# Performance work log

Measured on AMD Instinct MI355X. Metric: run time of the kernel, lower is better.

Reference implementation:

```python
import jax, jax.numpy as jnp
import numpy as np

N = 1_000_000      # level-0 points
M = 50_000         # level-1 superpoints
G = 16             # graphs in batch (norm_index groups)
DIMS = (32, 128, 64)
EPS = 1e-5
NEG_SLOPE = 0.01   # torch nn.LeakyReLU default


def graph_norm(x, idx, gamma, beta, num_graphs):
    """Per-graph batch norm ('graph' mode): normalize each feature channel
    using mean/var computed over the nodes of each graph (segment)."""
    cnt = jax.ops.segment_sum(jnp.ones((x.shape[0],), x.dtype), idx, num_segments=num_graphs)
    cnt = jnp.maximum(cnt, 1.0)[:, None]                       # [G,1]
    mean = jax.ops.segment_sum(x, idx, num_segments=num_graphs) / cnt      # [G,D]
    ex2 = jax.ops.segment_sum(x * x, idx, num_segments=num_graphs) / cnt   # [G,D]
    var = jnp.maximum(ex2 - mean * mean, 0.0)
    xn = (x - mean[idx]) * jax.lax.rsqrt(var[idx] + EPS)       # gather stats back to nodes
    return xn * gamma + beta


def setup_inputs() -> dict:
    key = jax.random.key(0)
    ks = jax.random.split(key, 8)
    d0, d1, d2 = DIMS
    x = jax.random.normal(ks[0], (N, d0), dtype=jnp.float32)
    W1 = jax.random.normal(ks[1], (d1, d0), dtype=jnp.float32) * (1.0 / np.sqrt(d0))
    b1 = jnp.zeros((d1,), jnp.float32)
    g1 = jnp.ones((d1,), jnp.float32)
    beta1 = jnp.zeros((d1,), jnp.float32)
    W2 = jax.random.normal(ks[2], (d2, d1), dtype=jnp.float32) * (1.0 / np.sqrt(d1))
    b2 = jnp.zeros((d2,), jnp.float32)
    g2 = jnp.ones((d2,), jnp.float32)
    beta2 = jnp.zeros((d2,), jnp.float32)
    norm_index = jnp.sort(jax.random.randint(ks[3], (N,), 0, G)).astype(jnp.int64)
    super_index = jax.random.randint(ks[4], (N,), 0, M).astype(jnp.int64)
    return {"x": x, "W1": W1, "b1": b1, "g1": g1, "beta1": beta1,
            "W2": W2, "b2": b2, "g2": g2, "beta2": beta2,
            "norm_index": norm_index, "super_index": super_index}


def reference(x, W1, b1, g1, beta1, W2, b2, g2, beta2, norm_index, super_index):
    # MLP layer 1: Linear -> graph BatchNorm -> LeakyReLU
    h = jnp.dot(x, W1.T) + b1                                  # [N,128]
    h = jax.nn.leaky_relu(graph_norm(h, norm_index, g1, beta1, G), NEG_SLOPE)
    # MLP layer 2
    h = jnp.dot(h, W2.T) + b2                                  # [N,64]
    h = jax.nn.leaky_relu(graph_norm(h, norm_index, g2, beta2, G), NEG_SLOPE)
    # level == 0: scatter-max pooling into level-1 superpoints
    out = jax.ops.segment_max(h, super_index, num_segments=M)  # [M,64]
    # torch_scatter leaves empty segments at 0; segment_max gives -inf
    out = jnp.where(jnp.isneginf(out), 0.0, out)
    return out
```

## Files before the change

kernel.cpp:

```cpp
#include <hip/hip_runtime.h>
#include <hip/hip_bf16.h>
#include <stdint.h>

#define NGRAPH 16
#define EPSV 1e-5f
#define SLOPE 0.01f

#define OFF_S1   0
#define OFF_CNT  512
#define OFF_SUM2 528
#define OFF_SQ2  1552
#define ZERO_SMALL 2576
#define OFF_A1   2576
#define OFF_C1   4624
#define OFF_A2   6672
#define OFF_C2   7696
#define OFF_M    16384
#define M_FLOATS 16384
#define H2_BYTE_OFF 65536

typedef __attribute__((ext_vector_type(4))) float f32x4;
typedef __attribute__((ext_vector_type(8))) short short8v;

__device__ __forceinline__ unsigned int enc_f32(float f) {
  unsigned int b = __float_as_uint(f);
  return (b & 0x80000000u) ? ~b : (b | 0x80000000u);
}
__device__ __forceinline__ unsigned int f2bf_bits(float f) {
  unsigned int u = __float_as_uint(f);
  unsigned int r = u + 0x7FFFu + ((u >> 16) & 1u);
  return r >> 16;
}
__device__ __forceinline__ float bfround(float f) {
  unsigned int u = __float_as_uint(f);
  unsigned int r = (u + 0x7FFFu + ((u >> 16) & 1u)) & 0xFFFF0000u;
  return __uint_as_float(r);
}

__global__ void k_zero_stats(float* __restrict__ ws) {
  int i = blockIdx.x * 256 + threadIdx.x;
  if (i < ZERO_SMALL) ws[i] = 0.0f;
  int j = i - ZERO_SMALL;
  if (j >= 0 && j < M_FLOATS) ws[OFF_M + j] = 0.0f;
}

__global__ void k_zero_ints(int* __restrict__ p, int n) {
  int i = blockIdx.x * 256 + threadIdx.x;
  if (i < n) p[i] = 0;
}

__global__ void k_init_out(unsigned int* __restrict__ out, int n) {
  int i = blockIdx.x * 256 + threadIdx.x;
  if (i < n) out[i] = 0u;
}

__global__ __launch_bounds__(256) void k1_mom(
    const float* __restrict__ x, const int* __restrict__ gidx,
    float* __restrict__ ws, int N) {
  const int tid = threadIdx.x;
  const int gw = blockIdx.x * 4 + (tid >> 6);
  const int l = tid & 63;
  const int bi = l >> 3, bj = l & 7;
  const bool diag = (bi == bj);
  const bool isL0 = (l == 0);
  const int nwaves = gridDim.x * 4;
  const int npw = (N + nwaves - 1) / nwaves;
  const int n0 = gw * npw;
  const int n1 = min(n0 + npw, N);

  float m00,m01,m02,m03,m10,m11,m12,m13,m20,m21,m22,m23,m30,m31,m32,m33;
  m00=m01=m02=m03=m10=m11=m12=m13=m20=m21=m22=m23=m30=m31=m32=m33=0.f;
  float sv0=0.f, sv1=0.f, sv2=0.f, sv3=0.f, cnt=0.f;
  int curg = -1;

  #pragma unroll 1
  for (int n = n0; n < n1; ++n) {
    int g = gidx[n];
    if (g != curg) {
      if (curg >= 0) {
        float* Mg = ws + OFF_M + curg * 1024 + bi * 4 * 32 + bj * 4;
        atomicAdd(Mg + 0*32 + 0, m00); atomicAdd(Mg + 0*32 + 1, m01);
        atomicAdd(Mg + 0*32 + 2, m02); atomicAdd(Mg + 0*32 + 3, m03);
        atomicAdd(Mg + 1*32 + 0, m10); atomicAdd(Mg + 1*32 + 1, m11);
        atomicAdd(Mg + 1*32 + 2, m12); atomicAdd(Mg + 1*32 + 3, m13);
        atomicAdd(Mg + 2*32 + 0, m20); atomicAdd(Mg + 2*32 + 1, m21);
        atomicAdd(Mg + 2*32 + 2, m22); atomicAdd(Mg + 2*32 + 3, m23);
        atomicAdd(Mg + 3*32 + 0, m30); atomicAdd(Mg + 3*32 + 1, m31);
        atomicAdd(Mg + 3*32 + 2, m32); atomicAdd(Mg + 3*32 + 3, m33);
        if (diag) {
          float* Sg = ws + OFF_S1 + curg * 32 + bi * 4;
          atomicAdd(Sg + 0, sv0); atomicAdd(Sg + 1, sv1);
          atomicAdd(Sg + 2, sv2); atomicAdd(Sg + 3, sv3);
        }
        if (isL0) atomicAdd(ws + OFF_CNT + curg, cnt);
      }
      curg = g;
      m00=m01=m02=m03=m10=m11=m12=m13=m20=m21=m22=m23=m30=m31=m32=m33=0.f;
      sv0=sv1=sv2=sv3=0.f; cnt=0.f;
    }
    const float* xr = x + (size_t)n * 32;
    float4 pi = *(const float4*)(xr + bi * 4);
    float4 pj = *(const float4*)(xr + bj * 4);
    float xi0 = bfround(pi.x), xi1 = bfround(pi.y), xi2 = bfround(pi.z), xi3 = bfround(pi.w);
    float xj0 = bfround(pj.x), xj1 = bfround(pj.y), xj2 = bfround(pj.z), xj3 = bfround(pj.w);
    m00 = fmaf(xi0,xj0,m00); m01 = fmaf(xi0,xj1,m01); m02 = fmaf(xi0,xj2,m02); m03 = fmaf(xi0,xj3,m03);
    m10 = fmaf(xi1,xj0,m10); m11 = fmaf(xi1,xj1,m11); m12 = fmaf(xi1,xj2,m12); m13 = fmaf(xi1,xj3,m13);
    m20 = fmaf(xi2,xj0,m20); m21 = fmaf(xi2,xj1,m21); m22 = fmaf(xi2,xj2,m22); m23 = fmaf(xi2,xj3,m23);
    m30 = fmaf(xi3,xj0,m30); m31 = fmaf(xi3,xj1,m31); m32 = fmaf(xi3,xj2,m32); m33 = fmaf(xi3,xj3,m33);
    if (diag) { sv0 += xi0; sv1 += xi1; sv2 += xi2; sv3 += xi3; }
    cnt += 1.f;
  }
  if (curg >= 0) {
    float* Mg = ws + OFF_M + curg * 1024 + bi * 4 * 32 + bj * 4;
    atomicAdd(Mg + 0*32 + 0, m00); atomicAdd(Mg + 0*32 + 1, m01);
    atomicAdd(Mg + 0*32 + 2, m02); atomicAdd(Mg + 0*32 + 3, m03);
    atomicAdd(Mg + 1*32 + 0, m10); atomicAdd(Mg + 1*32 + 1, m11);
    atomicAdd(Mg + 1*32 + 2, m12); atomicAdd(Mg + 1*32 + 3, m13);
    atomicAdd(Mg + 2*32 + 0, m20); atomicAdd(Mg + 2*32 + 1, m21);
    atomicAdd(Mg + 2*32 + 2, m22); atomicAdd(Mg + 2*32 + 3, m23);
    atomicAdd(Mg + 3*32 + 0, m30); atomicAdd(Mg + 3*32 + 1, m31);
    atomicAdd(Mg + 3*32 + 2, m32); atomicAdd(Mg + 3*32 + 3, m33);
    if (diag) {
      float* Sg = ws + OFF_S1 + curg * 32 + bi * 4;
      atomicAdd(Sg + 0, sv0); atomicAdd(Sg + 1, sv1);
      atomicAdd(Sg + 2, sv2); atomicAdd(Sg + 3, sv3);
    }
    if (isL0) atomicAdd(ws + OFF_CNT + curg, cnt);
  }
}

__global__ __launch_bounds__(128) void k2a_fin1(
    const float* __restrict__ W1, const float* __restrict__ b1,
    const float* __restrict__ g1, const float* __restrict__ be1,
    float* __restrict__ ws) {
  __shared__ float Ms[1024];
  __shared__ float ss[32];
  __shared__ float cs;
  const int g = blockIdx.x, c = threadIdx.x;
  for (int i = c; i < 1024; i += 128) Ms[i] = ws[OFF_M + g * 1024 + i];
  if (c < 32) ss[c] = ws[OFF_S1 + g * 32 + c];
  if (c == 0) cs = fmaxf(ws[OFF_CNT + g], 1.0f);
  __syncthreads();
  float w[32];
  #pragma unroll
  for (int k = 0; k < 32; ++k) w[k] = bfround(W1[c * 32 + k]);
  float dot = 0.f;
  #pragma unroll
  for (int k = 0; k < 32; ++k) dot = fmaf(w[k], ss[k], dot);
  float quad = 0.f;
  #pragma unroll 1
  for (int i = 0; i < 32; ++i) {
    const float* Mr = Ms + i * 32;
    float acc = 0.f;
    #pragma unroll
    for (int j = 0; j < 32; ++j) acc = fmaf(Mr[j], w[j], acc);
    quad = fmaf(w[i], acc, quad);
  }
  const float cnt = cs;
  const float bc = b1[c];
  const float mean = dot / cnt + bc;
  const float e2 = (quad + 2.f * bc * dot) / cnt + bc * bc;
  const float var = fmaxf(e2 - mean * mean, 0.0f);
  const float a = rsqrtf(var + EPSV) * g1[c];
  ws[OFF_A1 + g * 128 + c] = a;
  ws[OFF_C1 + g * 128 + c] = fmaf(a, bc - mean, be1[c]);
}

__global__ void k2_fin(float* __restrict__ ws, const float* __restrict__ gamma,
                       const float* __restrict__ beta, int D, int off_sum,
                       int off_sq, int off_a, int off_c) {
  int i = blockIdx.x * 256 + threadIdx.x;
  if (i >= NGRAPH * D) return;
  int g = i / D, c = i % D;
  float cnt  = fmaxf(ws[OFF_CNT + g], 1.0f);
  float mean = ws[off_sum + i] / cnt;
  float ex2  = ws[off_sq + i] / cnt;
  float var  = fmaxf(ex2 - mean * mean, 0.0f);
  float a = rsqrtf(var + EPSV) * gamma[c];
  ws[off_a + i] = a;
  ws[off_c + i] = fmaf(-mean, a, beta[c]);
}

__global__ __launch_bounds__(256) void k3_mfma(
    const float* __restrict__ x, const float* __restrict__ W1,
    const float* __restrict__ W2, const float* __restrict__ b2,
    const int* __restrict__ gidx, float* __restrict__ ws,
    unsigned short* __restrict__ h2out, int N, int ntiles, int tpb) {
  __shared__ float a1s[2048];
  __shared__ float c1s[2048];
  __shared__ __align__(16) unsigned short h1t[4][2048];
  const int tid = threadIdx.x;
  const int wv = tid >> 6;
  const int l = tid & 63;
  const int ln = l & 15;
  const int kq = l >> 4;

  for (int i = tid; i < 2048; i += 256) { a1s[i] = ws[OFF_A1 + i]; c1s[i] = ws[OFF_C1 + i]; }

  short8v w1f[8];
  #pragma unroll
  for (int t = 0; t < 8; ++t) {
    const float* wr = W1 + (size_t)(t * 16 + ln) * 32 + kq * 8;
    float4 p = *(const float4*)wr, q = *(const float4*)(wr + 4);
    short8v f;
    f[0] = (short)f2bf_bits(p.x); f[1] = (short)f2bf_bits(p.y);
    f[2] = (short)f2bf_bits(p.z); f[3] = (short)f2bf_bits(p.w);
    f[4] = (short)f2bf_bits(q.x); f[5] = (short)f2bf_bits(q.y);
    f[6] = (short)f2bf_bits(q.z); f[7] = (short)f2bf_bits(q.w);
    w1f[t] = f;
  }
  short8v w2f[4][4];
  #pragma unroll
  for (int ct = 0; ct < 4; ++ct)
    #pragma unroll
    for (int kt = 0; kt < 4; ++kt) {
      const float* wr = W2 + (size_t)(ct * 16 + ln) * 128 + kt * 32 + kq * 8;
      float4 p = *(const float4*)wr, q = *(const float4*)(wr + 4);
      short8v f;
      f[0] = (short)f2bf_bits(p.x); f[1] = (short)f2bf_bits(p.y);
      f[2] = (short)f2bf_bits(p.z); f[3] = (short)f2bf_bits(p.w);
      f[4] = (short)f2bf_bits(q.x); f[5] = (short)f2bf_bits(q.y);
      f[6] = (short)f2bf_bits(q.z); f[7] = (short)f2bf_bits(q.w);
      w2f[ct][kt] = f;
    }
  float b2v[4];
  #pragma unroll
  for (int ct = 0; ct < 4; ++ct) b2v[ct] = b2[ct * 16 + ln];
  __syncthreads();

  unsigned short* myt = &h1t[wv][0];
  const f32x4 zero4 = {0.f, 0.f, 0.f, 0.f};
  float s2[4] = {0.f, 0.f, 0.f, 0.f}, q2[4] = {0.f, 0.f, 0.f, 0.f};
  int curg2 = -1;

  const int t0 = blockIdx.x * tpb;
  const int t1 = min(t0 + tpb, ntiles);
  #pragma unroll 1
  for (int tb = t0; tb < t1; tb += 4) {
    const int tile = tb + wv;
    const bool act = (tile < t1);
    int gg[4] = {0, 0, 0, 0};
    if (act) {
      const int base = tile * 16;
      const int nodeA = min(base + ln, N - 1);
      const float* xr = x + (size_t)nodeA * 32 + kq * 8;
      float4 p = *(const float4*)xr, q = *(const float4*)(xr + 4);
      short8v af;
      af[0] = (short)f2bf_bits(p.x); af[1] = (short)f2bf_bits(p.y);
      af[2] = (short)f2bf_bits(p.z); af[3] = (short)f2bf_bits(p.w);
      af[4] = (short)f2bf_bits(q.x); af[5] = (short)f2bf_bits(q.y);
      af[6] = (short)f2bf_bits(q.z); af[7] = (short)f2bf_bits(q.w);
      f32x4 acc1[8];
      #pragma unroll
      for (int t = 0; t < 8; ++t)
        acc1[t] = __builtin_amdgcn_mfma_f32_16x16x32_bf16(af, w1f[t], zero4, 0, 0, 0);
      #pragma unroll
      for (int i = 0; i < 4; ++i)
        gg[i] = gidx[min(base + kq * 4 + i, N - 1)];
      #pragma unroll
      for (int t = 0; t < 8; ++t) {
        const int ct_ = t * 16 + ln;
        #pragma unroll
        for (int i = 0; i < 4; ++i) {
          const float a = a1s[gg[i] * 128 + ct_];
          const float cc = c1s[gg[i] * 128 + ct_];
          float v = fmaf(acc1[t][i], a, cc);
          v = v >= 0.f ? v : v * SLOPE;
          const int row = kq * 4 + i;
          const int byte = (row * 256 + ct_ * 2) ^ ((row & 7) << 4);
          *(unsigned short*)((char*)myt + byte) = (unsigned short)f2bf_bits(v);
        }
      }
    }
    __syncthreads();
    if (act) {
      const int base = tile * 16;
      short8v a2f[4];
      #pragma unroll
      for (int kt = 0; kt < 4; ++kt) {
        const int byte = (ln * 256 + kt * 64 + kq * 16) ^ ((ln & 7) << 4);
        a2f[kt] = *(const short8v*)((const char*)myt + byte);
      }
      f32x4 acc2[4];
      #pragma unroll
      for (int ct = 0; ct < 4; ++ct) {
        f32x4 a = zero4;
        #pragma unroll
        for (int kt = 0; kt < 4; ++kt)
          a = __builtin_amdgcn_mfma_f32_16x16x32_bf16(a2f[kt], w2f[ct][kt], a, 0, 0, 0);
        acc2[ct] = a;
      }
      #pragma unroll
      for (int i = 0; i < 4; ++i) {
        const int node = base + kq * 4 + i;
        if (node >= N) break;
        const int g = gg[i];
        if (g != curg2) {
          if (curg2 >= 0) {
            #pragma unroll
            for (int ct = 0; ct < 4; ++ct) {
              atomicAdd(ws + OFF_SUM2 + curg2 * 64 + ct * 16 + ln, s2[ct]);
              atomicAdd(ws + OFF_SQ2  + curg2 * 64 + ct * 16 + ln, q2[ct]);
            }
          }
          curg2 = g;
          #pragma unroll
          for (int ct = 0; ct < 4; ++ct) { s2[ct] = 0.f; q2[ct] = 0.f; }
        }
        #pragma unroll
        for (int ct = 0; ct < 4; ++ct) {
          const float v2 = acc2[ct][i] + b2v[ct];
          s2[ct] += v2; q2[ct] = fmaf(v2, v2, q2[ct]);
          h2out[(size_t)node * 64 + ct * 16 + ln] = (unsigned short)f2bf_bits(v2);
        }
      }
    }
  }
  if (curg2 >= 0) {
    #pragma unroll
    for (int ct = 0; ct < 4; ++ct) {
      atomicAdd(ws + OFF_SUM2 + curg2 * 64 + ct * 16 + ln, s2[ct]);
      atomicAdd(ws + OFF_SQ2  + curg2 * 64 + ct * 16 + ln, q2[ct]);
    }
  }
}

__global__ void k5a_hist(const int* __restrict__ sidx, int* __restrict__ hist, int N) {
  int n = blockIdx.x * 256 + threadIdx.x;
  if (n < N) atomicAdd(&hist[sidx[n]], 1);
}

__global__ __launch_bounds__(256) void k5b_scan(
    const int* __restrict__ hist, int* __restrict__ offsets,
    int* __restrict__ cursor, int M, int N) {
  __shared__ int part[256];
  const int tid = threadIdx.x;
  const int chunk = (M + 255) / 256;
  const int lo = min(tid * chunk, M), hi = min(lo + chunk, M);
  int s = 0;
  for (int i = lo; i < hi; ++i) s += hist[i];
  part[tid] = s;
  __syncthreads();
  if (tid == 0) {
    int run = 0;
    for (int i = 0; i < 256; ++i) { int v = part[i]; part[i] = run; run += v; }
  }
  __syncthreads();
  int run = part[tid];
  for (int i = lo; i < hi; ++i) {
    int v = hist[i];
    offsets[i] = run; cursor[i] = run; run += v;
  }
  if (tid == 255) offsets[M] = N;
}

__global__ void k5c_perm(const int* __restrict__ sidx, int* __restrict__ cursor,
                         int* __restrict__ perm, int N) {
  int n = blockIdx.x * 256 + threadIdx.x;
  if (n >= N) return;
  int sp = sidx[n];
  int pos = atomicAdd(&cursor[sp], 1);
  perm[pos] = n;
}

__global__ __launch_bounds__(256) void k5d_gather(
    const unsigned short* __restrict__ h2, const int* __restrict__ perm,
    const int* __restrict__ offsets, const int* __restrict__ gidx,
    const float* __restrict__ ws, float* __restrict__ out, int M) {
  __shared__ float a2s[1024], c2s[1024];
  const int tid = threadIdx.x;
  for (int i = tid; i < 1024; i += 256) { a2s[i] = ws[OFF_A2 + i]; c2s[i] = ws[OFF_C2 + i]; }
  __syncthreads();
  const int seg = blockIdx.x * 4 + (tid >> 6);
  if (seg >= M) return;
  const int lane = tid & 63;
  const int lo = offsets[seg], hi = offsets[seg + 1];
  float acc = -3.402823466e38f;
  #pragma unroll 1
  for (int i = lo; i < hi; ++i) {
    const int node = perm[i];
    const int g = gidx[node];
    const unsigned short hb = h2[(size_t)node * 64 + lane];
    const float v = __uint_as_float((unsigned int)hb << 16);
    float y = fmaf(v, a2s[g * 64 + lane], c2s[g * 64 + lane]);
    y = y >= 0.f ? y : y * SLOPE;
    acc = fmaxf(acc, y);
  }
  out[(size_t)seg * 64 + lane] = (hi > lo) ? acc : 0.0f;
}

__global__ __launch_bounds__(256) void k5_scatter(
    const unsigned int* __restrict__ h2, const int* __restrict__ gidx,
    const int* __restrict__ sidx, const float* __restrict__ ws,
    unsigned int* __restrict__ out, int N) {
  int t = blockIdx.x * 256 + threadIdx.x;
  int node = t >> 4;
  if (node >= N) return;
  int jq = t & 15, j = jq * 4;
  int g = gidx[node];
  int sp = sidx[node];
  float4 av = *(const float4*)(ws + OFF_A2 + g * 64 + j);
  float4 cv = *(const float4*)(ws + OFF_C2 + g * 64 + j);
  uint2 hv = *(const uint2*)(h2 + (size_t)node * 32 + jq * 2);
  float v0 = __uint_as_float(hv.x << 16);
  float v1 = __uint_as_float(hv.x & 0xFFFF0000u);
  float v2 = __uint_as_float(hv.y << 16);
  float v3 = __uint_as_float(hv.y & 0xFFFF0000u);
  v0 = fmaf(v0, av.x, cv.x); v0 = v0 >= 0.f ? v0 : v0 * SLOPE;
  v1 = fmaf(v1, av.y, cv.y); v1 = v1 >= 0.f ? v1 : v1 * SLOPE;
  v2 = fmaf(v2, av.z, cv.z); v2 = v2 >= 0.f ? v2 : v2 * SLOPE;
  v3 = fmaf(v3, av.w, cv.w); v3 = v3 >= 0.f ? v3 : v3 * SLOPE;
  unsigned int* o = out + (size_t)sp * 64 + j;
  atomicMax(o + 0, enc_f32(v0));
  atomicMax(o + 1, enc_f32(v1));
  atomicMax(o + 2, enc_f32(v2));
  atomicMax(o + 3, enc_f32(v3));
}

__global__ void k6_decode(unsigned int* __restrict__ o, int n) {
  int i = blockIdx.x * 256 + threadIdx.x;
  if (i >= n) return;
  unsigned int e = o[i];
  float f;
  if (e == 0u) f = 0.0f;
  else if (e & 0x80000000u) f = __uint_as_float(e ^ 0x80000000u);
  else f = __uint_as_float(~e);
  ((float*)o)[i] = f;
}

extern "C" void kernel_launch(void* const* d_in, const int* in_sizes, int n_in,
                              void* d_out, int out_size, void* d_ws, size_t ws_size,
                              hipStream_t stream) {
  const float* x   = (const float*)d_in[0];
  const float* W1  = (const float*)d_in[1];
  const float* b1  = (const float*)d_in[2];
  const float* g1  = (const float*)d_in[3];
  const float* be1 = (const float*)d_in[4];
  const float* W2  = (const float*)d_in[5];
  const float* b2  = (const float*)d_in[6];
  const float* g2  = (const float*)d_in[7];
  const float* be2 = (const float*)d_in[8];
  const int* gidx  = (const int*)d_in[9];
  const int* sidx  = (const int*)d_in[10];
  const int N = in_sizes[9];
  const int M = out_size / 64;
  float* ws = (float*)d_ws;
  unsigned short* h2 = (unsigned short*)((char*)d_ws + H2_BYTE_OFF);
  unsigned int* out_u = (unsigned int*)d_out;

  const size_t idx_off = (size_t)H2_BYTE_OFF + (size_t)N * 128;
  int* hist    = (int*)((char*)d_ws + idx_off);
  int* cursor  = hist + M;
  int* offsets = cursor + M;
  int* perm    = offsets + M + 1;
  const size_t needed_fast = idx_off + (size_t)(3 * M + 1 + N) * 4;
  const bool fast = (ws_size >= needed_fast);

  const int zthreads = ZERO_SMALL + M_FLOATS;
  hipLaunchKernelGGL(k_zero_stats, dim3((zthreads + 255) / 256), dim3(256), 0, stream, ws);
  hipLaunchKernelGGL(k1_mom, dim3(1024), dim3(256), 0, stream, x, gidx, ws, N);
  hipLaunchKernelGGL(k2a_fin1, dim3(NGRAPH), dim3(128), 0, stream, W1, b1, g1, be1, ws);
  const int ntiles = (N + 15) / 16;
  const int tpb = (ntiles + 1023) / 1024;
  const int k3blocks = (ntiles + tpb - 1) / tpb;
  hipLaunchKernelGGL(k3_mfma, dim3(k3blocks), dim3(256), 0, stream,
                     x, W1, W2, b2, gidx, ws, h2, N, ntiles, tpb);
  hipLaunchKernelGGL(k2_fin, dim3((NGRAPH * 64 + 255) / 256), dim3(256), 0, stream,
                     ws, g2, be2, 64, OFF_SUM2, OFF_SQ2, OFF_A2, OFF_C2);
  if (fast) {
    hipLaunchKernelGGL(k_zero_ints, dim3((M + 255) / 256), dim3(256), 0, stream, hist, M);
    hipLaunchKernelGGL(k5a_hist, dim3((N + 255) / 256), dim3(256), 0, stream, sidx, hist, N);
    hipLaunchKernelGGL(k5b_scan, dim3(1), dim3(256), 0, stream, hist, offsets, cursor, M, N);
    hipLaunchKernelGGL(k5c_perm, dim3((N + 255) / 256), dim3(256), 0, stream,
                       sidx, cursor, perm, N);
    hipLaunchKernelGGL(k5d_gather, dim3((M + 3) / 4), dim3(256), 0, stream,
                       h2, perm, offsets, gidx, ws, (float*)d_out, M);
  } else {
    hipLaunchKernelGGL(k_init_out, dim3((out_size + 255) / 256), dim3(256), 0, stream,
                       out_u, out_size);
    hipLaunchKernelGGL(k5_scatter, dim3((N * 16 + 255) / 256), dim3(256), 0, stream,
                       (const unsigned int*)h2, gidx, sidx, ws, out_u, N);
    hipLaunchKernelGGL(k6_decode, dim3((out_size + 255) / 256), dim3(256), 0, stream,
                       out_u, out_size);
  }
}
```

Baseline: 1.133 ms.

## Prefetch next rows in moment, MFMA and gather loops; drop block syncs

Several changes land together. The moment kernel and the gather kernel now software-prefetch the next row, index and perm entry one or two iterations ahead to hide load latency. The MFMA kernel gives each wave its own contiguous run of tiles, which removes the per-iteration __syncthreads, and it also prefetches the next tile. The graph id is packed into the perm entries so the gather loop no longer reads gidx per node. The zeroing kernels are merged into one, and the histogram, scan and perm kernels are moved earlier in the stream. This costs some extra registers and redundant clamped loads at the ends of each range.

```diff
diff --git a/kernel.cpp b/kernel.cpp
--- a/kernel.cpp
+++ b/kernel.cpp
@@ -37,16 +37,11 @@
   return __uint_as_float(r);
 }
 
-__global__ void k_zero_stats(float* __restrict__ ws) {
+__global__ void k_zero_all(float* __restrict__ ws, int* __restrict__ hist, int M) {
   int i = blockIdx.x * 256 + threadIdx.x;
   if (i < ZERO_SMALL) ws[i] = 0.0f;
-  int j = i - ZERO_SMALL;
-  if (j >= 0 && j < M_FLOATS) ws[OFF_M + j] = 0.0f;
-}
-
-__global__ void k_zero_ints(int* __restrict__ p, int n) {
-  int i = blockIdx.x * 256 + threadIdx.x;
-  if (i < n) p[i] = 0;
+  if (i < M_FLOATS) ws[OFF_M + i] = 0.0f;
+  if (i < M) hist[i] = 0;
 }
 
 __global__ void k_init_out(unsigned int* __restrict__ out, int n) {
@@ -73,42 +68,49 @@
   float sv0=0.f, sv1=0.f, sv2=0.f, sv3=0.f, cnt=0.f;
   int curg = -1;
 
-  #pragma unroll 1
-  for (int n = n0; n < n1; ++n) {
-    int g = gidx[n];
-    if (g != curg) {
-      if (curg >= 0) {
-        float* Mg = ws + OFF_M + curg * 1024 + bi * 4 * 32 + bj * 4;
-        atomicAdd(Mg + 0*32 + 0, m00); atomicAdd(Mg + 0*32 + 1, m01);
-        atomicAdd(Mg + 0*32 + 2, m02); atomicAdd(Mg + 0*32 + 3, m03);
-        atomicAdd(Mg + 1*32 + 0, m10); atomicAdd(Mg + 1*32 + 1, m11);
-        atomicAdd(Mg + 1*32 + 2, m12); atomicAdd(Mg + 1*32 + 3, m13);
-        atomicAdd(Mg + 2*32 + 0, m20); atomicAdd(Mg + 2*32 + 1, m21);
-        atomicAdd(Mg + 2*32 + 2, m22); atomicAdd(Mg + 2*32 + 3, m23);
-        atomicAdd(Mg + 3*32 + 0, m30); atomicAdd(Mg + 3*32 + 1, m31);
-        atomicAdd(Mg + 3*32 + 2, m32); atomicAdd(Mg + 3*32 + 3, m33);
-        if (diag) {
-          float* Sg = ws + OFF_S1 + curg * 32 + bi * 4;
-          atomicAdd(Sg + 0, sv0); atomicAdd(Sg + 1, sv1);
-          atomicAdd(Sg + 2, sv2); atomicAdd(Sg + 3, sv3);
+  if (n0 < n1) {
+    const int nlast = n1 - 1;
+    int g = gidx[n0];
+    float4 pi = *(const float4*)(x + (size_t)n0 * 32 + bi * 4);
+    float4 pj = *(const float4*)(x + (size_t)n0 * 32 + bj * 4);
+    #pragma unroll 1
+    for (int n = n0; n < n1; ++n) {
+      const int nn = min(n + 1, nlast);
+      const int g2 = gidx[nn];
+      float4 pi2 = *(const float4*)(x + (size_t)nn * 32 + bi * 4);
+      float4 pj2 = *(const float4*)(x + (size_t)nn * 32 + bj * 4);
+      if (g != curg) {
+        if (curg >= 0) {
+          float* Mg = ws + OFF_M + curg * 1024 + bi * 4 * 32 + bj * 4;
+          atomicAdd(Mg + 0*32 + 0, m00); atomicAdd(Mg + 0*32 + 1, m01);
+          atomicAdd(Mg + 0*32 + 2, m02); atomicAdd(Mg + 0*32 + 3, m03);
+          atomicAdd(Mg + 1*32 + 0, m10); atomicAdd(Mg + 1*32 + 1, m11);
+          atomicAdd(Mg + 1*32 + 2, m12); atomicAdd(Mg + 1*32 + 3, m13);
+          atomicAdd(Mg + 2*32 + 0, m20); atomicAdd(Mg + 2*32 + 1, m21);
+          atomicAdd(Mg + 2*32 + 2, m22); atomicAdd(Mg + 2*32 + 3, m23);
+          atomicAdd(Mg + 3*32 + 0, m30); atomicAdd(Mg + 3*32 + 1, m31);
+          atomicAdd(Mg + 3*32 + 2, m32); atomicAdd(Mg + 3*32 + 3, m33);
+          if (diag) {
+            float* Sg = ws + OFF_S1 + curg * 32 + bi * 4;
+            atomicAdd(Sg + 0, sv0); atomicAdd(Sg + 1, sv1);
+            atomicAdd(Sg + 2, sv2); atomicAdd(Sg + 3, sv3);
+          }
+          if (isL0) atomicAdd(ws + OFF_CNT + curg, cnt);
         }
-        if (isL0) atomicAdd(ws + OFF_CNT + curg, cnt);
+        curg = g;
+        m00=m01=m02=m03=m10=m11=m12=m13=m20=m21=m22=m23=m30=m31=m32=m33=0.f;
+        sv0=sv1=sv2=sv3=0.f; cnt=0.f;
       }
-      curg = g;
-      m00=m01=m02=m03=m10=m11=m12=m13=m20=m21=m22=m23=m30=m31=m32=m33=0.f;
-      sv0=sv1=sv2=sv3=0.f; cnt=0.f;
-    }
-    const float* xr = x + (size_t)n * 32;
-    float4 pi = *(const float4*)(xr + bi * 4);
-    float4 pj = *(const float4*)(xr + bj * 4);
-    float xi0 = bfround(pi.x), xi1 = bfround(pi.y), xi2 = bfround(pi.z), xi3 = bfround(pi.w);
-    float xj0 = bfround(pj.x), xj1 = bfround(pj.y), xj2 = bfround(pj.z), xj3 = bfround(pj.w);
-    m00 = fmaf(xi0,xj0,m00); m01 = fmaf(xi0,xj1,m01); m02 = fmaf(xi0,xj2,m02); m03 = fmaf(xi0,xj3,m03);
-    m10 = fmaf(xi1,xj0,m10); m11 = fmaf(xi1,xj1,m11); m12 = fmaf(xi1,xj2,m12); m13 = fmaf(xi1,xj3,m13);
-    m20 = fmaf(xi2,xj0,m20); m21 = fmaf(xi2,xj1,m21); m22 = fmaf(xi2,xj2,m22); m23 = fmaf(xi2,xj3,m23);
-    m30 = fmaf(xi3,xj0,m30); m31 = fmaf(xi3,xj1,m31); m32 = fmaf(xi3,xj2,m32); m33 = fmaf(xi3,xj3,m33);
-    if (diag) { sv0 += xi0; sv1 += xi1; sv2 += xi2; sv3 += xi3; }
-    cnt += 1.f;
+      float xi0 = bfround(pi.x), xi1 = bfround(pi.y), xi2 = bfround(pi.z), xi3 = bfround(pi.w);
+      float xj0 = bfround(pj.x), xj1 = bfround(pj.y), xj2 = bfround(pj.z), xj3 = bfround(pj.w);
+      m00 = fmaf(xi0,xj0,m00); m01 = fmaf(xi0,xj1,m01); m02 = fmaf(xi0,xj2,m02); m03 = fmaf(xi0,xj3,m03);
+      m10 = fmaf(xi1,xj0,m10); m11 = fmaf(xi1,xj1,m11); m12 = fmaf(xi1,xj2,m12); m13 = fmaf(xi1,xj3,m13);
+      m20 = fmaf(xi2,xj0,m20); m21 = fmaf(xi2,xj1,m21); m22 = fmaf(xi2,xj2,m22); m23 = fmaf(xi2,xj3,m23);
+      m30 = fmaf(xi3,xj0,m30); m31 = fmaf(xi3,xj1,m31); m32 = fmaf(xi3,xj2,m32); m33 = fmaf(xi3,xj3,m33);
+      if (diag) { sv0 += xi0; sv1 += xi1; sv2 += xi2; sv3 += xi3; }
+      cnt += 1.f;
+      pi = pi2; pj = pj2; g = g2;
+    }
   }
   if (curg >= 0) {
     float* Mg = ws + OFF_M + curg * 1024 + bi * 4 * 32 + bj * 4;
@@ -185,7 +187,7 @@
     const float* __restrict__ x, const float* __restrict__ W1,
     const float* __restrict__ W2, const float* __restrict__ b2,
     const int* __restrict__ gidx, float* __restrict__ ws,
-    unsigned short* __restrict__ h2out, int N, int ntiles, int tpb) {
+    unsigned short* __restrict__ h2out, int N, int ntiles, int tpw) {
   __shared__ float a1s[2048];
   __shared__ float c1s[2048];
   __shared__ __align__(16) unsigned short h1t[4][2048];
@@ -228,99 +230,111 @@
   for (int ct = 0; ct < 4; ++ct) b2v[ct] = b2[ct * 16 + ln];
   __syncthreads();
 
+  const int gw = blockIdx.x * 4 + wv;
+  const int t0 = gw * tpw;
+  const int t1 = min(t0 + tpw, ntiles);
+  if (t0 >= t1) return;
+
   unsigned short* myt = &h1t[wv][0];
   const f32x4 zero4 = {0.f, 0.f, 0.f, 0.f};
-  float s2[4] = {0.f, 0.f, 0.f, 0.f}, q2[4] = {0.f, 0.f, 0.f, 0.f};
+  float s2[4] = {0.f, 0.f, 0.f, 0.f}, q2a[4] = {0.f, 0.f, 0.f, 0.f};
   int curg2 = -1;
 
-  const int t0 = blockIdx.x * tpb;
-  const int t1 = min(t0 + tpb, ntiles);
+  float4 p, q;
+  int gg[4];
+  {
+    const int base = t0 * 16;
+    const float* xr = x + (size_t)min(base + ln, N - 1) * 32 + kq * 8;
+    p = *(const float4*)xr; q = *(const float4*)(xr + 4);
+    #pragma unroll
+    for (int i = 0; i < 4; ++i) gg[i] = gidx[min(base + kq * 4 + i, N - 1)];
+  }
+
   #pragma unroll 1
-  for (int tb = t0; tb < t1; tb += 4) {
-    const int tile = tb + wv;
-    const bool act = (tile < t1);
-    int gg[4] = {0, 0, 0, 0};
-    if (act) {
-      const int base = tile * 16;
-      const int nodeA = min(base + ln, N - 1);
-      const float* xr = x + (size_t)nodeA * 32 + kq * 8;
-      float4 p = *(const float4*)xr, q = *(const float4*)(xr + 4);
-      short8v af;
-      af[0] = (short)f2bf_bits(p.x); af[1] = (short)f2bf_bits(p.y);
-      af[2] = (short)f2bf_bits(p.z); af[3] = (short)f2bf_bits(p.w);
-      af[4] = (short)f2bf_bits(q.x); af[5] = (short)f2bf_bits(q.y);
-      af[6] = (short)f2bf_bits(q.z); af[7] = (short)f2bf_bits(q.w);
-      f32x4 acc1[8];
+  for (int t = t0; t < t1; ++t) {
+    const int base = t * 16;
+    float4 p2, q2;
+    int gg2[4];
+    {
+      const int nb = min(t + 1, t1 - 1) * 16;
+      const float* xr = x + (size_t)min(nb + ln, N - 1) * 32 + kq * 8;
+      p2 = *(const float4*)xr; q2 = *(const float4*)(xr + 4);
       #pragma unroll
-      for (int t = 0; t < 8; ++t)
-        acc1[t] = __builtin_amdgcn_mfma_f32_16x16x32_bf16(af, w1f[t], zero4, 0, 0, 0);
+      for (int i = 0; i < 4; ++i) gg2[i] = gidx[min(nb + kq * 4 + i, N - 1)];
+    }
+    short8v af;
+    af[0] = (short)f2bf_bits(p.x); af[1] = (short)f2bf_bits(p.y);
+    af[2] = (short)f2bf_bits(p.z); af[3] = (short)f2bf_bits(p.w);
+    af[4] = (short)f2bf_bits(q.x); af[5] = (short)f2bf_bits(q.y);
+    af[6] = (short)f2bf_bits(q.z); af[7] = (short)f2bf_bits(q.w);
+    f32x4 acc1[8];
+    #pragma unroll
+    for (int tt = 0; tt < 8; ++tt)
+      acc1[tt] = __builtin_amdgcn_mfma_f32_16x16x32_bf16(af, w1f[tt], zero4, 0, 0, 0);
+    #pragma unroll
+    for (int tt = 0; tt < 8; ++tt) {
+      const int ct_ = tt * 16 + ln;
       #pragma unroll
-      for (int i = 0; i < 4; ++i)
-        gg[i] = gidx[min(base + kq * 4 + i, N - 1)];
+      for (int i = 0; i < 4; ++i) {
+        const float a = a1s[gg[i] * 128 + ct_];
+        const float cc = c1s[gg[i] * 128 + ct_];
+        float v = fmaf(acc1[tt][i], a, cc);
+        v = v >= 0.f ? v : v * SLOPE;
+        const int row = kq * 4 + i;
+        const int byte = (row * 256 + ct_ * 2) ^ ((row & 7) << 4);
+        *(unsigned short*)((char*)myt + byte) = (unsigned short)f2bf_bits(v);
+      }
+    }
+    asm volatile("s_waitcnt lgkmcnt(0)" ::: "memory");
+    __builtin_amdgcn_sched_barrier(0);
+    short8v a2f[4];
+    #pragma unroll
+    for (int kt = 0; kt < 4; ++kt) {
+      const int byte = (ln * 256 + kt * 64 + kq * 16) ^ ((ln & 7) << 4);
+      a2f[kt] = *(const short8v*)((const char*)myt + byte);
+    }
+    f32x4 acc2[4];
+    #pragma unroll
+    for (int ct = 0; ct < 4; ++ct) {
+      f32x4 a = zero4;
       #pragma unroll
-      for (int t = 0; t < 8; ++t) {
-        const int ct_ = t * 16 + ln;
+      for (int kt = 0; kt < 4; ++kt)
+        a = __builtin_amdgcn_mfma_f32_16x16x32_bf16(a2f[kt], w2f[ct][kt], a, 0, 0, 0);
+      acc2[ct] = a;
+    }
+    #pragma unroll
+    for (int i = 0; i < 4; ++i) {
+      const int node = base + kq * 4 + i;
+      if (node >= N) break;
+      const int g = gg[i];
+      if (g != curg2) {
+        if (curg2 >= 0) {
+          #pragma unroll
+          for (int ct = 0; ct < 4; ++ct) {
+            atomicAdd(ws + OFF_SUM2 + curg2 * 64 + ct * 16 + ln, s2[ct]);
+            atomicAdd(ws + OFF_SQ2  + curg2 * 64 + ct * 16 + ln, q2a[ct]);
+          }
+        }
+        curg2 = g;
         #pragma unroll
-        for (int i = 0; i < 4; ++i) {
-          const float a = a1s[gg[i] * 128 + ct_];
-          const float cc = c1s[gg[i] * 128 + ct_];
-          float v = fmaf(acc1[t][i], a, cc);
-          v = v >= 0.f ? v : v * SLOPE;
-          const int row = kq * 4 + i;
-          const int byte = (row * 256 + ct_ * 2) ^ ((row & 7) << 4);
-          *(unsigned short*)((char*)myt + byte) = (unsigned short)f2bf_bits(v);
-        }
+        for (int ct = 0; ct < 4; ++ct) { s2[ct] = 0.f; q2a[ct] = 0.f; }
       }
-    }
-    __syncthreads();
-    if (act) {
-      const int base = tile * 16;
-      short8v a2f[4];
-      #pragma unroll
-      for (int kt = 0; kt < 4; ++kt) {
-        const int byte = (ln * 256 + kt * 64 + kq * 16) ^ ((ln & 7) << 4);
-        a2f[kt] = *(const short8v*)((const char*)myt + byte);
-      }
-      f32x4 acc2[4];
       #pragma unroll
       for (int ct = 0; ct < 4; ++ct) {
-        f32x4 a = zero4;
-        #pragma unroll
-        for (int kt = 0; kt < 4; ++kt)
-          a = __builtin_amdgcn_mfma_f32_16x16x32_bf16(a2f[kt], w2f[ct][kt], a, 0, 0, 0);
-        acc2[ct] = a;
+        const float v2 = acc2[ct][i] + b2v[ct];
+        s2[ct] += v2; q2a[ct] = fmaf(v2, v2, q2a[ct]);
+        h2out[(size_t)node * 64 + ct * 16 + ln] = (unsigned short)f2bf_bits(v2);
       }
-      #pragma unroll
-      for (int i = 0; i < 4; ++i) {
-        const int node = base + kq * 4 + i;
-        if (node >= N) break;
-        const int g = gg[i];
-        if (g != curg2) {
-          if (curg2 >= 0) {
-            #pragma unroll
-            for (int ct = 0; ct < 4; ++ct) {
-              atomicAdd(ws + OFF_SUM2 + curg2 * 64 + ct * 16 + ln, s2[ct]);
-              atomicAdd(ws + OFF_SQ2  + curg2 * 64 + ct * 16 + ln, q2[ct]);
-            }
-          }
-          curg2 = g;
-          #pragma unroll
-          for (int ct = 0; ct < 4; ++ct) { s2[ct] = 0.f; q2[ct] = 0.f; }
-        }
-        #pragma unroll
-        for (int ct = 0; ct < 4; ++ct) {
-          const float v2 = acc2[ct][i] + b2v[ct];
-          s2[ct] += v2; q2[ct] = fmaf(v2, v2, q2[ct]);
-          h2out[(size_t)node * 64 + ct * 16 + ln] = (unsigned short)f2bf_bits(v2);
-        }
-      }
-    }
+    }
+    p = p2; q = q2;
+    #pragma unroll
+    for (int i = 0; i < 4; ++i) gg[i] = gg2[i];
   }
   if (curg2 >= 0) {
     #pragma unroll
     for (int ct = 0; ct < 4; ++ct) {
       atomicAdd(ws + OFF_SUM2 + curg2 * 64 + ct * 16 + ln, s2[ct]);
-      atomicAdd(ws + OFF_SQ2  + curg2 * 64 + ct * 16 + ln, q2[ct]);
+      atomicAdd(ws + OFF_SQ2  + curg2 * 64 + ct * 16 + ln, q2a[ct]);
     }
   }
 }
@@ -354,19 +368,19 @@
   if (tid == 255) offsets[M] = N;
 }
 
-__global__ void k5c_perm(const int* __restrict__ sidx, int* __restrict__ cursor,
-                         int* __restrict__ perm, int N) {
+__global__ void k5c_perm(const int* __restrict__ sidx, const int* __restrict__ gidx,
+                         int* __restrict__ cursor, int* __restrict__ perm, int N) {
   int n = blockIdx.x * 256 + threadIdx.x;
   if (n >= N) return;
   int sp = sidx[n];
   int pos = atomicAdd(&cursor[sp], 1);
-  perm[pos] = n;
+  perm[pos] = (n << 4) | (gidx[n] & 15);
 }
 
 __global__ __launch_bounds__(256) void k5d_gather(
     const unsigned short* __restrict__ h2, const int* __restrict__ perm,
-    const int* __restrict__ offsets, const int* __restrict__ gidx,
-    const float* __restrict__ ws, float* __restrict__ out, int M) {
+    const int* __restrict__ offsets, const float* __restrict__ ws,
+    float* __restrict__ out, int M) {
   __shared__ float a2s[1024], c2s[1024];
   const int tid = threadIdx.x;
   for (int i = tid; i < 1024; i += 256) { a2s[i] = ws[OFF_A2 + i]; c2s[i] = ws[OFF_C2 + i]; }
@@ -376,15 +390,22 @@
   const int lane = tid & 63;
   const int lo = offsets[seg], hi = offsets[seg + 1];
   float acc = -3.402823466e38f;
-  #pragma unroll 1
-  for (int i = lo; i < hi; ++i) {
-    const int node = perm[i];
-    const int g = gidx[node];
-    const unsigned short hb = h2[(size_t)node * 64 + lane];
-    const float v = __uint_as_float((unsigned int)hb << 16);
-    float y = fmaf(v, a2s[g * 64 + lane], c2s[g * 64 + lane]);
-    y = y >= 0.f ? y : y * SLOPE;
-    acc = fmaxf(acc, y);
+  if (hi > lo) {
+    const int last = hi - 1;
+    int pc = perm[lo];
+    unsigned short hc = h2[(size_t)(pc >> 4) * 64 + lane];
+    int pn = perm[min(lo + 1, last)];
+    #pragma unroll 1
+    for (int i = lo; i < hi; ++i) {
+      const unsigned short hn = h2[(size_t)(pn >> 4) * 64 + lane];
+      const int pn2 = perm[min(i + 2, last)];
+      const int g = pc & 15;
+      const float v = __uint_as_float((unsigned int)hc << 16);
+      float y = fmaf(v, a2s[g * 64 + lane], c2s[g * 64 + lane]);
+      y = y >= 0.f ? y : y * SLOPE;
+      acc = fmaxf(acc, y);
+      pc = pn; hc = hn; pn = pn2;
+    }
   }
   out[(size_t)seg * 64 + lane] = (hi > lo) ? acc : 0.0f;
 }
@@ -456,25 +477,28 @@
   const size_t needed_fast = idx_off + (size_t)(3 * M + 1 + N) * 4;
   const bool fast = (ws_size >= needed_fast);
 
-  const int zthreads = ZERO_SMALL + M_FLOATS;
-  hipLaunchKernelGGL(k_zero_stats, dim3((zthreads + 255) / 256), dim3(256), 0, stream, ws);
+  const int zmax = (M_FLOATS > M ? M_FLOATS : M);
+  hipLaunchKernelGGL(k_zero_all, dim3((zmax + 255) / 256), dim3(256), 0, stream,
+                     ws, hist, fast ? M : 0);
   hipLaunchKernelGGL(k1_mom, dim3(1024), dim3(256), 0, stream, x, gidx, ws, N);
   hipLaunchKernelGGL(k2a_fin1, dim3(NGRAPH), dim3(128), 0, stream, W1, b1, g1, be1, ws);
+  if (fast) {
+    hipLaunchKernelGGL(k5a_hist, dim3((N + 255) / 256), dim3(256), 0, stream, sidx, hist, N);
+    hipLaunchKernelGGL(k5b_scan, dim3(1), dim3(256), 0, stream, hist, offsets, cursor, M, N);
+    hipLaunchKernelGGL(k5c_perm, dim3((N + 255) / 256), dim3(256), 0, stream,
+                       sidx, gidx, cursor, perm, N);
+  }
   const int ntiles = (N + 15) / 16;
-  const int tpb = (ntiles + 1023) / 1024;
-  const int k3blocks = (ntiles + tpb - 1) / tpb;
+  const int NW = 4096;
+  const int tpw = (ntiles + NW - 1) / NW;
+  const int k3blocks = (ntiles + 4 * tpw - 1) / (4 * tpw);
   hipLaunchKernelGGL(k3_mfma, dim3(k3blocks), dim3(256), 0, stream,
-                     x, W1, W2, b2, gidx, ws, h2, N, ntiles, tpb);
+                     x, W1, W2, b2, gidx, ws, h2, N, ntiles, tpw);
   hipLaunchKernelGGL(k2_fin, dim3((NGRAPH * 64 + 255) / 256), dim3(256), 0, stream,
                      ws, g2, be2, 64, OFF_SUM2, OFF_SQ2, OFF_A2, OFF_C2);
   if (fast) {
-    hipLaunchKernelGGL(k_zero_ints, dim3((M + 255) / 256), dim3(256), 0, stream, hist, M);
-    hipLaunchKernelGGL(k5a_hist, dim3((N + 255) / 256), dim3(256), 0, stream, sidx, hist, N);
-    hipLaunchKernelGGL(k5b_scan, dim3(1), dim3(256), 0, stream, hist, offsets, cursor, M, N);
-    hipLaunchKernelGGL(k5c_perm, dim3((N + 255) / 256), dim3(256), 0, stream,
-                       sidx, cursor, perm, N);
     hipLaunchKernelGGL(k5d_gather, dim3((M + 3) / 4), dim3(256), 0, stream,
-                       h2, perm, offsets, gidx, ws, (float*)d_out, M);
+                       h2, perm, offsets, ws, (float*)d_out, M);
   } else {
     hipLaunchKernelGGL(k_init_out, dim3((out_size + 255) / 256), dim3(256), 0, stream,
                        out_u, out_size);
```

Result: faster. 1.031 ms (-9.0%).
